# Performance work log

Hardware: AMD Instinct MI355X
Metric: run time of the kernel (lower is better)

Reference implementation:

```python
import jax, jax.numpy as jnp
import numpy as np

B, S, DIN, DOUT = 4, 2048, 4096, 4096
DR, TR = 512, 64  # decomposition_rank, training_rank


def setup_inputs() -> dict:
    key = jax.random.key(0)
    ks = jax.random.split(key, 7)
    return {
        "x": jax.random.normal(ks[0], (B, S, DIN), dtype=jnp.float32),
        "u_t": jax.random.normal(ks[1], (DOUT, TR), dtype=jnp.float32) * 0.02,
        "s": jax.random.uniform(ks[2], (DR,), dtype=jnp.float32),
        "v_t": jax.random.normal(ks[3], (TR, DIN), dtype=jnp.float32) * 0.02,
        "u_d": jax.random.normal(ks[4], (DOUT, DR - TR), dtype=jnp.float32) * 0.02,
        "v_d": jax.random.normal(ks[5], (DR - TR, DIN), dtype=jnp.float32) * 0.02,
        "bias": jax.random.normal(ks[6], (DOUT,), dtype=jnp.float32) * 0.02,
    }


def reference(x, u_t, s, v_t, u_d, v_d, bias):
    tr = u_t.shape[1]  # training_rank
    # Faithful to original: materialize full [out, in] weight from scaled factors.
    siva_train = (u_t * s[:tr]) @ v_t            # [out, in]
    siva_dec = (u_d * s[tr:]) @ v_d              # [out, in]
    weight = siva_train + siva_dec               # [out, in]
    # F.linear: x @ weight.T + bias
    return jnp.einsum('bsi,oi->bso', x, weight) + bias
```

## Files before the change

kernel.cpp:

```cpp
#include <hip/hip_runtime.h>

typedef __bf16 bf16;
typedef unsigned int u32;
typedef __attribute__((ext_vector_type(4))) float f32x4;
typedef __attribute__((ext_vector_type(8))) __bf16 bf16x8;
typedef __attribute__((ext_vector_type(4))) __bf16 bf16x4;

#define MFMA(a, b, c) __builtin_amdgcn_mfma_f32_16x16x32_bf16((a), (b), (c), 0, 0, 0)

#define DIN 4096
#define DOUT 4096
#define DR 512

__device__ __forceinline__ void gll16(const void* g, void* l) {
  __builtin_amdgcn_global_load_lds((const __attribute__((address_space(1))) u32*)g,
                                   (__attribute__((address_space(3))) u32*)l, 16, 0, 0);
}

__global__ __launch_bounds__(256) void prep_v_kernel(const float* __restrict__ vt,
                                                     const float* __restrict__ vd,
                                                     bf16* __restrict__ Vb) {
  int idx = blockIdx.x * 256 + threadIdx.x;
  int e = idx * 4;
  int r = e >> 12, c = e & 4095;
  const float* src = (r < 64) ? (vt + ((size_t)r << 12) + c) : (vd + ((size_t)(r - 64) << 12) + c);
  float4 v = *reinterpret_cast<const float4*>(src);
  bf16x4 o = {(bf16)v.x, (bf16)v.y, (bf16)v.z, (bf16)v.w};
  *reinterpret_cast<bf16x4*>(Vb + e) = o;
}

__global__ __launch_bounds__(256) void prep_u_kernel(const float* __restrict__ ut,
                                                     const float* __restrict__ ud,
                                                     const float* __restrict__ s,
                                                     bf16* __restrict__ Ub) {
  int idx = blockIdx.x * 256 + threadIdx.x;
  int o = idx >> 7;
  int rr = (idx & 127) * 4;
  const float* src = (rr < 64) ? (ut + (size_t)o * 64 + rr) : (ud + (size_t)o * 448 + (rr - 64));
  float4 v = *reinterpret_cast<const float4*>(src);
  float4 sv = *reinterpret_cast<const float4*>(s + rr);
  bf16x4 ov = {(bf16)(v.x * sv.x), (bf16)(v.y * sv.y), (bf16)(v.z * sv.z), (bf16)(v.w * sv.w)};
  *reinterpret_cast<bf16x4*>(Ub + (size_t)o * DR + rr) = ov;
}

__global__ __launch_bounds__(256) void gemm1_kernel(const float* __restrict__ X,
                                                    const bf16* __restrict__ Vb,
                                                    bf16* __restrict__ T) {
  __shared__ alignas(16) bf16 As[2][64 * 40];
  __shared__ alignas(16) bf16 Bs[2][128 * 32];

  const int tid = threadIdx.x;
  const int bid = blockIdx.x;
  const int xcd = bid & 7, slot = bid >> 3;
  const int mt = xcd * 16 + (slot >> 2), nt = slot & 3;
  const int m0 = mt * 64, n0 = nt * 128;

  const int wid = tid >> 6, lane = tid & 63;
  const int wr = wid >> 1, wc = wid & 1;
  const int lr = lane & 15, kg = lane >> 4;
  const int ks = kg ^ ((lr >> 1) & 3);

  const int arow = tid >> 2, aseg = tid & 3;
  const float* aG = X + (size_t)(m0 + arow) * DIN + aseg * 8;
  const int aWoff = arow * 40 + aseg * 8;

  const int bs_ = (lane & 3) ^ ((lane >> 3) & 3);
  const int rl = lane >> 2;
  const int ci0 = wid * 2, ci1 = wid * 2 + 1;
  const bf16* bG0 = Vb + (size_t)(n0 + ci0 * 16 + rl) * DIN + bs_ * 8;
  const bf16* bG1 = Vb + (size_t)(n0 + ci1 * 16 + rl) * DIN + bs_ * 8;

  f32x4 acc[2][4];
  const f32x4 z = {0.f, 0.f, 0.f, 0.f};
#pragma unroll
  for (int i = 0; i < 2; ++i)
#pragma unroll
    for (int j = 0; j < 4; ++j) acc[i][j] = z;

  {
    float4 v0 = *reinterpret_cast<const float4*>(aG);
    float4 v1 = *reinterpret_cast<const float4*>(aG + 4);
    bf16x8 w = {(bf16)v0.x, (bf16)v0.y, (bf16)v0.z, (bf16)v0.w,
                (bf16)v1.x, (bf16)v1.y, (bf16)v1.z, (bf16)v1.w};
    *reinterpret_cast<bf16x8*>(&As[0][aWoff]) = w;
    gll16(bG0, &Bs[0][ci0 * 512]);
    gll16(bG1, &Bs[0][ci1 * 512]);
  }
  __syncthreads();

  const int NT = DIN / 32;
  for (int kt = 0; kt < NT; ++kt) {
    const int cur = kt & 1;
    const bool pre = (kt + 1 < NT);
    float4 v0, v1;
    if (pre) {
      const float* ag = aG + (size_t)(kt + 1) * 32;
      v0 = *reinterpret_cast<const float4*>(ag);
      v1 = *reinterpret_cast<const float4*>(ag + 4);
      bf16* dB = (bf16*)Bs[cur ^ 1];
      gll16(bG0 + (size_t)(kt + 1) * 32, dB + ci0 * 512);
      gll16(bG1 + (size_t)(kt + 1) * 32, dB + ci1 * 512);
    }
    bf16x8 afr[2], bfr[4];
#pragma unroll
    for (int mi = 0; mi < 2; ++mi)
      afr[mi] = *reinterpret_cast<const bf16x8*>(&As[cur][(wr * 32 + mi * 16 + lr) * 40 + kg * 8]);
#pragma unroll
    for (int ni = 0; ni < 4; ++ni)
      bfr[ni] = *reinterpret_cast<const bf16x8*>(&Bs[cur][(wc * 64 + ni * 16 + lr) * 32 + ks * 8]);
#pragma unroll
    for (int mi = 0; mi < 2; ++mi)
#pragma unroll
      for (int ni = 0; ni < 4; ++ni)
        acc[mi][ni] = MFMA(afr[mi], bfr[ni], acc[mi][ni]);
    if (pre) {
      bf16x8 w = {(bf16)v0.x, (bf16)v0.y, (bf16)v0.z, (bf16)v0.w,
                  (bf16)v1.x, (bf16)v1.y, (bf16)v1.z, (bf16)v1.w};
      *reinterpret_cast<bf16x8*>(&As[cur ^ 1][aWoff]) = w;
    }
    __syncthreads();
  }

#pragma unroll
  for (int mi = 0; mi < 2; ++mi) {
    const int rbase = m0 + wr * 32 + mi * 16 + kg * 4;
#pragma unroll
    for (int ni = 0; ni < 4; ++ni) {
      const int c = n0 + wc * 64 + ni * 16 + lr;
      f32x4 a = acc[mi][ni];
#pragma unroll
      for (int j = 0; j < 4; ++j)
        T[(size_t)(rbase + j) * DR + c] = (bf16)a[j];
    }
  }
}

__global__ __launch_bounds__(256) void gemm2_kernel(const bf16* __restrict__ T,
                                                    const bf16* __restrict__ Ub,
                                                    const float* __restrict__ bias,
                                                    float* __restrict__ Out) {
  __shared__ alignas(16) bf16 As[2][128 * 32];
  __shared__ alignas(16) bf16 Bs[2][128 * 32];

  const int tid = threadIdx.x;
  const int id = ((blockIdx.x & 7) << 8) | (blockIdx.x >> 3);
  const int mt = id >> 5, nt = id & 31;
  const int m0 = mt * 128, n0 = nt * 128;

  const int wid = tid >> 6, lane = tid & 63;
  const int wr = wid >> 1, wc = wid & 1;
  const int lr = lane & 15, kg = lane >> 4;
  const int ks = kg ^ ((lr >> 1) & 3);

  const int bs_ = (lane & 3) ^ ((lane >> 3) & 3);
  const int rl = lane >> 2;
  const int ci0 = wid * 2, ci1 = wid * 2 + 1;
  const bf16* aG0 = T + (size_t)(m0 + ci0 * 16 + rl) * DR + bs_ * 8;
  const bf16* aG1 = T + (size_t)(m0 + ci1 * 16 + rl) * DR + bs_ * 8;
  const bf16* bG0 = Ub + (size_t)(n0 + ci0 * 16 + rl) * DR + bs_ * 8;
  const bf16* bG1 = Ub + (size_t)(n0 + ci1 * 16 + rl) * DR + bs_ * 8;

  f32x4 acc[4][4];
  const f32x4 z = {0.f, 0.f, 0.f, 0.f};
#pragma unroll
  for (int i = 0; i < 4; ++i)
#pragma unroll
    for (int j = 0; j < 4; ++j) acc[i][j] = z;

  {
    gll16(aG0, &As[0][ci0 * 512]);
    gll16(aG1, &As[0][ci1 * 512]);
    gll16(bG0, &Bs[0][ci0 * 512]);
    gll16(bG1, &Bs[0][ci1 * 512]);
  }
  __syncthreads();

  const int NT = DR / 32;
  for (int kt = 0; kt < NT; ++kt) {
    const int cur = kt & 1;
    const bool pre = (kt + 1 < NT);
    if (pre) {
      const size_t koff = (size_t)(kt + 1) * 32;
      bf16* dA = (bf16*)As[cur ^ 1];
      bf16* dB = (bf16*)Bs[cur ^ 1];
      gll16(aG0 + koff, dA + ci0 * 512);
      gll16(aG1 + koff, dA + ci1 * 512);
      gll16(bG0 + koff, dB + ci0 * 512);
      gll16(bG1 + koff, dB + ci1 * 512);
    }
    bf16x8 afr[4], bfr[4];
#pragma unroll
    for (int mi = 0; mi < 4; ++mi)
      afr[mi] = *reinterpret_cast<const bf16x8*>(&As[cur][(wr * 64 + mi * 16 + lr) * 32 + ks * 8]);
#pragma unroll
    for (int ni = 0; ni < 4; ++ni)
      bfr[ni] = *reinterpret_cast<const bf16x8*>(&Bs[cur][(wc * 64 + ni * 16 + lr) * 32 + ks * 8]);
#pragma unroll
    for (int mi = 0; mi < 4; ++mi)
#pragma unroll
      for (int ni = 0; ni < 4; ++ni)
        acc[mi][ni] = MFMA(afr[mi], bfr[ni], acc[mi][ni]);
    __syncthreads();
  }

#pragma unroll
  for (int ni = 0; ni < 4; ++ni) {
    const int c = n0 + wc * 64 + ni * 16 + lr;
    const float bv = bias[c];
#pragma unroll
    for (int mi = 0; mi < 4; ++mi) {
      const int rbase = m0 + wr * 64 + mi * 16 + kg * 4;
      f32x4 a = acc[mi][ni];
#pragma unroll
      for (int j = 0; j < 4; ++j)
        Out[(size_t)(rbase + j) * DOUT + c] = a[j] + bv;
    }
  }
}

extern "C" void kernel_launch(void* const* d_in, const int* in_sizes, int n_in,
                              void* d_out, int out_size, void* d_ws, size_t ws_size,
                              hipStream_t stream) {
  const float* x = (const float*)d_in[0];
  const float* u_t = (const float*)d_in[1];
  const float* s = (const float*)d_in[2];
  const float* v_t = (const float*)d_in[3];
  const float* u_d = (const float*)d_in[4];
  const float* v_d = (const float*)d_in[5];
  const float* bias = (const float*)d_in[6];
  float* out = (float*)d_out;

  bf16* Vb = (bf16*)d_ws;
  bf16* Ub = (bf16*)((char*)d_ws + (4u << 20));
  bf16* T = (bf16*)((char*)d_ws + (8u << 20));

  hipLaunchKernelGGL(prep_v_kernel, dim3(2048), dim3(256), 0, stream, v_t, v_d, Vb);
  hipLaunchKernelGGL(prep_u_kernel, dim3(2048), dim3(256), 0, stream, u_t, u_d, s, Ub);
  hipLaunchKernelGGL(gemm1_kernel, dim3(512), dim3(256), 0, stream, x, Vb, T);
  hipLaunchKernelGGL(gemm2_kernel, dim3(2048), dim3(256), 0, stream, T, Ub, bias, out);
}
```

Baseline: 391.1 us.

## Deepen both GEMMs to four-stage LDS pipelines with explicit waitcnt and single barrier

Both GEMM kernels move from double-buffered LDS with two __syncthreads per step to a 4-buffer ring. Loads are issued two k-steps ahead, and in gemm1 the fp32 X loads are issued three steps ahead in registers. Manual s_waitcnt vmcnt/lgkmcnt and sched_barrier replace the compiler-inserted waits so each iteration needs one barrier. The X tile in LDS switches from padded rows to an XOR swizzle. This is meant to hide global memory latency and remove barrier stalls, at the cost of more LDS and register use plus fragile hand-written wait counts.

New measurement: 387.6 us. About the same (-0.9%).

```diff
diff --git a/kernel.cpp b/kernel.cpp
--- a/kernel.cpp
+++ b/kernel.cpp
@@ -6,7 +6,7 @@
 typedef __attribute__((ext_vector_type(8))) __bf16 bf16x8;
 typedef __attribute__((ext_vector_type(4))) __bf16 bf16x4;
 
-#define MFMA(a, b, c) __builtin_amdgcn_mfma_f32_16x16x32_bf16((a), (b), (c), 0, 0, 0)
+#define MFMA_(a, b, c) __builtin_amdgcn_mfma_f32_16x16x32_bf16((a), (b), (c), 0, 0, 0)
 
 #define DIN 4096
 #define DOUT 4096
@@ -16,6 +16,12 @@
   __builtin_amdgcn_global_load_lds((const __attribute__((address_space(1))) u32*)g,
                                    (__attribute__((address_space(3))) u32*)l, 16, 0, 0);
 }
+
+#define FENCE() asm volatile("" ::: "memory")
+#define SCHEDB() __builtin_amdgcn_sched_barrier(0)
+#define WAITVM8() do { SCHEDB(); asm volatile("s_waitcnt vmcnt(8)" ::: "memory"); } while (0)
+#define WAITLGKM0() asm volatile("s_waitcnt lgkmcnt(0)" ::: "memory")
+#define BARRIER() do { FENCE(); __builtin_amdgcn_s_barrier(); SCHEDB(); } while (0)
 
 __global__ __launch_bounds__(256) void prep_v_kernel(const float* __restrict__ vt,
                                                      const float* __restrict__ vd,
@@ -46,11 +52,10 @@
 __global__ __launch_bounds__(256) void gemm1_kernel(const float* __restrict__ X,
                                                     const bf16* __restrict__ Vb,
                                                     bf16* __restrict__ T) {
-  __shared__ alignas(16) bf16 As[2][64 * 40];
-  __shared__ alignas(16) bf16 Bs[2][128 * 32];
-
-  const int tid = threadIdx.x;
-  const int bid = blockIdx.x;
+  __shared__ alignas(16) bf16 As[4 * 2048];
+  __shared__ alignas(16) bf16 Bs[4 * 4096];
+
+  const int tid = threadIdx.x, bid = blockIdx.x;
   const int xcd = bid & 7, slot = bid >> 3;
   const int mt = xcd * 16 + (slot >> 2), nt = slot & 3;
   const int m0 = mt * 64, n0 = nt * 128;
@@ -60,15 +65,21 @@
   const int lr = lane & 15, kg = lane >> 4;
   const int ks = kg ^ ((lr >> 1) & 3);
 
-  const int arow = tid >> 2, aseg = tid & 3;
-  const float* aG = X + (size_t)(m0 + arow) * DIN + aseg * 8;
-  const int aWoff = arow * 40 + aseg * 8;
-
-  const int bs_ = (lane & 3) ^ ((lane >> 3) & 3);
-  const int rl = lane >> 2;
-  const int ci0 = wid * 2, ci1 = wid * 2 + 1;
-  const bf16* bG0 = Vb + (size_t)(n0 + ci0 * 16 + rl) * DIN + bs_ * 8;
-  const bf16* bG1 = Vb + (size_t)(n0 + ci1 * 16 + rl) * DIN + bs_ * 8;
+  const int arow = tid >> 2, asl = tid & 3;
+  const int aphys = asl ^ ((arow >> 1) & 3);
+  const float* aG = X + (size_t)(m0 + arow) * DIN + asl * 8;
+  const int awoff = (arow * 4 + aphys) * 8;
+
+  const int c0 = wid * 2, c1 = wid * 2 + 1;
+  const int srcsl = (lane & 3) ^ ((lane >> 3) & 3);
+  const bf16* bG0 = Vb + (size_t)(n0 + c0 * 16 + (lane >> 2)) * DIN + srcsl * 8;
+  const bf16* bG1 = Vb + (size_t)(n0 + c1 * 16 + (lane >> 2)) * DIN + srcsl * 8;
+
+  int aoff[2], boff[4];
+#pragma unroll
+  for (int mi = 0; mi < 2; ++mi) aoff[mi] = ((wr * 32 + mi * 16 + lr) * 4 + ks) * 8;
+#pragma unroll
+  for (int ni = 0; ni < 4; ++ni) boff[ni] = ((wc * 64 + ni * 16 + lr) * 4 + ks) * 8;
 
   f32x4 acc[2][4];
   const f32x4 z = {0.f, 0.f, 0.f, 0.f};
@@ -77,49 +88,64 @@
 #pragma unroll
     for (int j = 0; j < 4; ++j) acc[i][j] = z;
 
+  float4 rA[4][2];
+
+  rA[0][0] = *reinterpret_cast<const float4*>(aG);
+  rA[0][1] = *reinterpret_cast<const float4*>(aG + 4);
+  SCHEDB();
+  gll16(bG0, &Bs[0 * 4096 + c0 * 512]);
+  gll16(bG1, &Bs[0 * 4096 + c1 * 512]);
+  rA[1][0] = *reinterpret_cast<const float4*>(aG + 32);
+  rA[1][1] = *reinterpret_cast<const float4*>(aG + 36);
+  SCHEDB();
+  gll16(bG0 + 32, &Bs[1 * 4096 + c0 * 512]);
+  gll16(bG1 + 32, &Bs[1 * 4096 + c1 * 512]);
+  rA[2][0] = *reinterpret_cast<const float4*>(aG + 64);
+  rA[2][1] = *reinterpret_cast<const float4*>(aG + 68);
+  WAITVM8();
   {
-    float4 v0 = *reinterpret_cast<const float4*>(aG);
-    float4 v1 = *reinterpret_cast<const float4*>(aG + 4);
+    float4 v0 = rA[0][0], v1 = rA[0][1];
     bf16x8 w = {(bf16)v0.x, (bf16)v0.y, (bf16)v0.z, (bf16)v0.w,
                 (bf16)v1.x, (bf16)v1.y, (bf16)v1.z, (bf16)v1.w};
-    *reinterpret_cast<bf16x8*>(&As[0][aWoff]) = w;
-    gll16(bG0, &Bs[0][ci0 * 512]);
-    gll16(bG1, &Bs[0][ci1 * 512]);
-  }
-  __syncthreads();
-
-  const int NT = DIN / 32;
-  for (int kt = 0; kt < NT; ++kt) {
-    const int cur = kt & 1;
-    const bool pre = (kt + 1 < NT);
-    float4 v0, v1;
-    if (pre) {
-      const float* ag = aG + (size_t)(kt + 1) * 32;
-      v0 = *reinterpret_cast<const float4*>(ag);
-      v1 = *reinterpret_cast<const float4*>(ag + 4);
-      bf16* dB = (bf16*)Bs[cur ^ 1];
-      gll16(bG0 + (size_t)(kt + 1) * 32, dB + ci0 * 512);
-      gll16(bG1 + (size_t)(kt + 1) * 32, dB + ci1 * 512);
-    }
-    bf16x8 afr[2], bfr[4];
-#pragma unroll
-    for (int mi = 0; mi < 2; ++mi)
-      afr[mi] = *reinterpret_cast<const bf16x8*>(&As[cur][(wr * 32 + mi * 16 + lr) * 40 + kg * 8]);
-#pragma unroll
-    for (int ni = 0; ni < 4; ++ni)
-      bfr[ni] = *reinterpret_cast<const bf16x8*>(&Bs[cur][(wc * 64 + ni * 16 + lr) * 32 + ks * 8]);
-#pragma unroll
-    for (int mi = 0; mi < 2; ++mi)
-#pragma unroll
-      for (int ni = 0; ni < 4; ++ni)
-        acc[mi][ni] = MFMA(afr[mi], bfr[ni], acc[mi][ni]);
-    if (pre) {
-      bf16x8 w = {(bf16)v0.x, (bf16)v0.y, (bf16)v0.z, (bf16)v0.w,
-                  (bf16)v1.x, (bf16)v1.y, (bf16)v1.z, (bf16)v1.w};
-      *reinterpret_cast<bf16x8*>(&As[cur ^ 1][aWoff]) = w;
-    }
-    __syncthreads();
-  }
+    *reinterpret_cast<bf16x8*>(&As[0 * 2048 + awoff]) = w;
+  }
+
+#define G1_BODY(t, RB, WB, PB, SW, SP)                                               \
+  do {                                                                               \
+    const int kt2 = ((t) + 2 < 128) ? (t) + 2 : 127;                                 \
+    const int kt3 = ((t) + 3 < 128) ? (t) + 3 : 127;                                 \
+    gll16(bG0 + (size_t)kt2 * 32, &Bs[(PB) * 4096 + c0 * 512]);                      \
+    gll16(bG1 + (size_t)kt2 * 32, &Bs[(PB) * 4096 + c1 * 512]);                      \
+    rA[SP][0] = *reinterpret_cast<const float4*>(aG + (size_t)kt3 * 32);             \
+    rA[SP][1] = *reinterpret_cast<const float4*>(aG + (size_t)kt3 * 32 + 4);         \
+    WAITVM8();                                              \
+    {                                                                                \
+      float4 v0 = rA[SW][0], v1 = rA[SW][1];                                         \
+      bf16x8 w = {(bf16)v0.x, (bf16)v0.y, (bf16)v0.z, (bf16)v0.w,                    \
+                  (bf16)v1.x, (bf16)v1.y, (bf16)v1.z, (bf16)v1.w};                   \
+      *reinterpret_cast<bf16x8*>(&As[(WB) * 2048 + awoff]) = w;                      \
+    }                                                                                \
+    WAITLGKM0();                                                                     \
+    BARRIER();                                                                       \
+    bf16x8 afr[2], bfr[4];                                                           \
+    afr[0] = *reinterpret_cast<const bf16x8*>(&As[(RB) * 2048 + aoff[0]]);           \
+    afr[1] = *reinterpret_cast<const bf16x8*>(&As[(RB) * 2048 + aoff[1]]);           \
+    bfr[0] = *reinterpret_cast<const bf16x8*>(&Bs[(RB) * 4096 + boff[0]]);           \
+    bfr[1] = *reinterpret_cast<const bf16x8*>(&Bs[(RB) * 4096 + boff[1]]);           \
+    bfr[2] = *reinterpret_cast<const bf16x8*>(&Bs[(RB) * 4096 + boff[2]]);           \
+    bfr[3] = *reinterpret_cast<const bf16x8*>(&Bs[(RB) * 4096 + boff[3]]);           \
+    _Pragma("unroll") for (int mi = 0; mi < 2; ++mi)                                 \
+        _Pragma("unroll") for (int ni = 0; ni < 4; ++ni)                             \
+            acc[mi][ni] = MFMA_(afr[mi], bfr[ni], acc[mi][ni]);                      \
+  } while (0)
+
+  for (int tb = 0; tb < 128; tb += 4) {
+    G1_BODY(tb + 0, 0, 1, 2, 1, 3);
+    G1_BODY(tb + 1, 1, 2, 3, 2, 0);
+    G1_BODY(tb + 2, 2, 3, 0, 3, 1);
+    G1_BODY(tb + 3, 3, 0, 1, 0, 2);
+  }
+#undef G1_BODY
 
 #pragma unroll
   for (int mi = 0; mi < 2; ++mi) {
@@ -135,12 +161,12 @@
   }
 }
 
-__global__ __launch_bounds__(256) void gemm2_kernel(const bf16* __restrict__ T,
+__global__ __launch_bounds__(256) void gemm2_kernel(const bf16* __restrict__ Tt,
                                                     const bf16* __restrict__ Ub,
                                                     const float* __restrict__ bias,
                                                     float* __restrict__ Out) {
-  __shared__ alignas(16) bf16 As[2][128 * 32];
-  __shared__ alignas(16) bf16 Bs[2][128 * 32];
+  __shared__ alignas(16) bf16 As[4 * 4096];
+  __shared__ alignas(16) bf16 Bs[4 * 4096];
 
   const int tid = threadIdx.x;
   const int id = ((blockIdx.x & 7) << 8) | (blockIdx.x >> 3);
@@ -152,13 +178,18 @@
   const int lr = lane & 15, kg = lane >> 4;
   const int ks = kg ^ ((lr >> 1) & 3);
 
-  const int bs_ = (lane & 3) ^ ((lane >> 3) & 3);
-  const int rl = lane >> 2;
-  const int ci0 = wid * 2, ci1 = wid * 2 + 1;
-  const bf16* aG0 = T + (size_t)(m0 + ci0 * 16 + rl) * DR + bs_ * 8;
-  const bf16* aG1 = T + (size_t)(m0 + ci1 * 16 + rl) * DR + bs_ * 8;
-  const bf16* bG0 = Ub + (size_t)(n0 + ci0 * 16 + rl) * DR + bs_ * 8;
-  const bf16* bG1 = Ub + (size_t)(n0 + ci1 * 16 + rl) * DR + bs_ * 8;
+  const int c0 = wid * 2, c1 = wid * 2 + 1;
+  const int srcsl = (lane & 3) ^ ((lane >> 3) & 3);
+  const bf16* aG0 = Tt + (size_t)(m0 + c0 * 16 + (lane >> 2)) * DR + srcsl * 8;
+  const bf16* aG1 = Tt + (size_t)(m0 + c1 * 16 + (lane >> 2)) * DR + srcsl * 8;
+  const bf16* bG0 = Ub + (size_t)(n0 + c0 * 16 + (lane >> 2)) * DR + srcsl * 8;
+  const bf16* bG1 = Ub + (size_t)(n0 + c1 * 16 + (lane >> 2)) * DR + srcsl * 8;
+
+  int aoff[4], boff[4];
+#pragma unroll
+  for (int mi = 0; mi < 4; ++mi) aoff[mi] = ((wr * 64 + mi * 16 + lr) * 4 + ks) * 8;
+#pragma unroll
+  for (int ni = 0; ni < 4; ++ni) boff[ni] = ((wc * 64 + ni * 16 + lr) * 4 + ks) * 8;
 
   f32x4 acc[4][4];
   const f32x4 z = {0.f, 0.f, 0.f, 0.f};
@@ -167,41 +198,43 @@
 #pragma unroll
     for (int j = 0; j < 4; ++j) acc[i][j] = z;
 
-  {
-    gll16(aG0, &As[0][ci0 * 512]);
-    gll16(aG1, &As[0][ci1 * 512]);
-    gll16(bG0, &Bs[0][ci0 * 512]);
-    gll16(bG1, &Bs[0][ci1 * 512]);
-  }
-  __syncthreads();
-
-  const int NT = DR / 32;
-  for (int kt = 0; kt < NT; ++kt) {
-    const int cur = kt & 1;
-    const bool pre = (kt + 1 < NT);
-    if (pre) {
-      const size_t koff = (size_t)(kt + 1) * 32;
-      bf16* dA = (bf16*)As[cur ^ 1];
-      bf16* dB = (bf16*)Bs[cur ^ 1];
-      gll16(aG0 + koff, dA + ci0 * 512);
-      gll16(aG1 + koff, dA + ci1 * 512);
-      gll16(bG0 + koff, dB + ci0 * 512);
-      gll16(bG1 + koff, dB + ci1 * 512);
-    }
-    bf16x8 afr[4], bfr[4];
-#pragma unroll
-    for (int mi = 0; mi < 4; ++mi)
-      afr[mi] = *reinterpret_cast<const bf16x8*>(&As[cur][(wr * 64 + mi * 16 + lr) * 32 + ks * 8]);
-#pragma unroll
-    for (int ni = 0; ni < 4; ++ni)
-      bfr[ni] = *reinterpret_cast<const bf16x8*>(&Bs[cur][(wc * 64 + ni * 16 + lr) * 32 + ks * 8]);
-#pragma unroll
-    for (int mi = 0; mi < 4; ++mi)
-#pragma unroll
-      for (int ni = 0; ni < 4; ++ni)
-        acc[mi][ni] = MFMA(afr[mi], bfr[ni], acc[mi][ni]);
-    __syncthreads();
-  }
+  gll16(aG0, &As[0 * 4096 + c0 * 512]);
+  gll16(aG1, &As[0 * 4096 + c1 * 512]);
+  gll16(bG0, &Bs[0 * 4096 + c0 * 512]);
+  gll16(bG1, &Bs[0 * 4096 + c1 * 512]);
+  SCHEDB();
+  gll16(aG0 + 32, &As[1 * 4096 + c0 * 512]);
+  gll16(aG1 + 32, &As[1 * 4096 + c1 * 512]);
+  gll16(bG0 + 32, &Bs[1 * 4096 + c0 * 512]);
+  gll16(bG1 + 32, &Bs[1 * 4096 + c1 * 512]);
+  SCHEDB();
+
+#define G2_BODY(t, RB, PB)                                                           \
+  do {                                                                               \
+    const int kt2 = ((t) + 2 < 16) ? (t) + 2 : 15;                                   \
+    gll16(aG0 + (size_t)kt2 * 32, &As[(PB) * 4096 + c0 * 512]);                      \
+    gll16(aG1 + (size_t)kt2 * 32, &As[(PB) * 4096 + c1 * 512]);                      \
+    gll16(bG0 + (size_t)kt2 * 32, &Bs[(PB) * 4096 + c0 * 512]);                      \
+    gll16(bG1 + (size_t)kt2 * 32, &Bs[(PB) * 4096 + c1 * 512]);                      \
+    WAITVM8();                                                      \
+    BARRIER();                                                                       \
+    bf16x8 afr[4], bfr[4];                                                           \
+    _Pragma("unroll") for (int mi = 0; mi < 4; ++mi)                                 \
+        afr[mi] = *reinterpret_cast<const bf16x8*>(&As[(RB) * 4096 + aoff[mi]]);     \
+    _Pragma("unroll") for (int ni = 0; ni < 4; ++ni)                                 \
+        bfr[ni] = *reinterpret_cast<const bf16x8*>(&Bs[(RB) * 4096 + boff[ni]]);     \
+    _Pragma("unroll") for (int mi = 0; mi < 4; ++mi)                                 \
+        _Pragma("unroll") for (int ni = 0; ni < 4; ++ni)                             \
+            acc[mi][ni] = MFMA_(afr[mi], bfr[ni], acc[mi][ni]);                      \
+  } while (0)
+
+  for (int tb = 0; tb < 16; tb += 4) {
+    G2_BODY(tb + 0, 0, 2);
+    G2_BODY(tb + 1, 1, 3);
+    G2_BODY(tb + 2, 2, 0);
+    G2_BODY(tb + 3, 3, 1);
+  }
+#undef G2_BODY
 
 #pragma unroll
   for (int ni = 0; ni < 4; ++ni) {
```
